# Performance work log

Measured on AMD Instinct MI355X. Metric: run time of the kernel, lower is better.

The kernel has to match this reference:

```python
import jax, jax.numpy as jnp
import numpy as np


def setup_inputs() -> dict:
    key = jax.random.key(0)
    k1, k2 = jax.random.split(key)
    B, D, H, W = 16, 256, 32, 32
    K = 2048
    z = jax.random.normal(k1, (B, D, H, W), dtype=jnp.float32)
    # EmbeddingEMA init: uniform(-1/K, 1/K); plain randn scaled works as a stand-in param
    codebook = jax.random.uniform(k2, (K, D), dtype=jnp.float32,
                                  minval=-1.0 / K, maxval=1.0 / K)
    return {"z": z, "codebook": codebook}


def reference(z, codebook):
    # z: (B, D, H, W) -> (B, H, W, D) -> (n, D)   [normalize == 'none' path]
    B, D, H, W = z.shape
    z_flat = jnp.transpose(z, (0, 2, 3, 1)).reshape(-1, D)          # (n, D)
    z_norm = z_flat
    codebook_norm = codebook                                         # (K, D)

    # squared L2 distance: ||z||^2 + ||c||^2 - 2 z c^T   -> (n, K)
    distance = (jnp.sum(z_norm * z_norm, axis=1, keepdims=True)
                + jnp.sum(codebook_norm * codebook_norm, axis=1)
                - 2.0 * jnp.matmul(z_norm, codebook_norm.T))

    vq_indices = jnp.argmin(distance, axis=1)                        # (n,)
    z_q = codebook_norm[vq_indices]                                  # gather (n, D)

    # straight-through estimator (standard VQ forward output)
    z_q_st = z_norm + jax.lax.stop_gradient(z_q - z_norm)
    out = z_q_st.reshape(B, H, W, D).transpose(0, 3, 1, 2)           # (B, D, H, W)
    return out
```

## Files before the change

### kernel.cpp

```cpp
#include <hip/hip_runtime.h>
#include <stdint.h>


#define D_    256
#define K_    2048
#define HW_   1024
#define MT    64
#define NT    256
#define KT    16
#define SPLIT 4
#define KS    (K_ / SPLIT)
#define CST   256
#define BUFSZ (KT * CST)
#define NPH   ((KS / NT) * KT)
#define NPIX  16384

__device__ __forceinline__ void gload16(const float* g, float* l) {
    auto* gp = reinterpret_cast<const __attribute__((address_space(1))) uint32_t*>(
        reinterpret_cast<uintptr_t>(g));
    auto* lp = reinterpret_cast<__attribute__((address_space(3))) uint32_t*>(
        reinterpret_cast<uintptr_t>(l));
    __builtin_amdgcn_global_load_lds(gp, lp, 16, 0, 0);
}

__device__ __forceinline__ float pw8(const float r[8]) {
    float t01 = __fadd_rn(r[0], r[1]);
    float t23 = __fadd_rn(r[2], r[3]);
    float L   = __fadd_rn(t01, t23);
    float t45 = __fadd_rn(r[4], r[5]);
    float t67 = __fadd_rn(r[6], r[7]);
    float R   = __fadd_rn(t45, t67);
    return __fadd_rn(L, R);
}

__global__ __launch_bounds__(256) void prep_k(const float* __restrict__ z,
                                              const float* __restrict__ cb,
                                              float* __restrict__ ct,
                                              float* __restrict__ An,
                                              float* __restrict__ Bn) {
    __shared__ float t[64][65];
    int tid = threadIdx.x;
    int bx  = blockIdx.x;
    if (bx < 128) {
        int k0 = (bx & 31) << 6;
        int d0 = (bx >> 5) << 6;
        #pragma unroll
        for (int it = 0; it < 4; ++it) {
            int u  = (it << 8) + tid;
            int kk = u >> 4;
            int dd = (u & 15) << 2;
            float4 v = *reinterpret_cast<const float4*>(
                cb + (size_t)(k0 + kk) * D_ + d0 + dd);
            t[kk][dd + 0] = v.x; t[kk][dd + 1] = v.y;
            t[kk][dd + 2] = v.z; t[kk][dd + 3] = v.w;
        }
        __syncthreads();
        #pragma unroll
        for (int it = 0; it < 4; ++it) {
            int u  = (it << 8) + tid;
            int dd = u >> 4;
            int kk = (u & 15) << 2;
            float4 o;
            o.x = t[kk + 0][dd]; o.y = t[kk + 1][dd];
            o.z = t[kk + 2][dd]; o.w = t[kk + 3][dd];
            *reinterpret_cast<float4*>(ct + (size_t)(d0 + dd) * K_ + k0 + kk) = o;
        }
    } else if (bx < 136) {
        int row = (bx - 128) * 256 + tid;
        const float4* p = reinterpret_cast<const float4*>(cb + (size_t)row * D_);
        float rA[8], rB[8];
        #pragma unroll
        for (int j = 0; j < 8; ++j) { rA[j] = 0.f; rB[j] = 0.f; }
        #pragma unroll
        for (int q = 0; q < 64; ++q) {
            float4 v = p[q];
            float pv[4] = {__fmul_rn(v.x, v.x), __fmul_rn(v.y, v.y),
                           __fmul_rn(v.z, v.z), __fmul_rn(v.w, v.w)};
            if (q < 32) {
                #pragma unroll
                for (int l = 0; l < 4; ++l)
                    rA[(4 * q + l) & 7] = __fadd_rn(rA[(4 * q + l) & 7], pv[l]);
            } else {
                #pragma unroll
                for (int l = 0; l < 4; ++l)
                    rB[(4 * q + l) & 7] = __fadd_rn(rB[(4 * q + l) & 7], pv[l]);
            }
        }
        Bn[row] = __fadd_rn(pw8(rA), pw8(rB));
    } else {
        int blk = bx - 136;
        int b   = blk >> 2;
        int hw0 = (blk & 3) << 8;
        const float* zb = z + (size_t)b * (D_ * HW_) + hw0 + tid;
        float rA[8], rB[8];
        #pragma unroll
        for (int j = 0; j < 8; ++j) { rA[j] = 0.f; rB[j] = 0.f; }
        #pragma unroll 8
        for (int d = 0; d < 128; ++d) {
            float v = zb[(size_t)d * HW_];
            rA[d & 7] = __fadd_rn(rA[d & 7], __fmul_rn(v, v));
        }
        #pragma unroll 8
        for (int d = 128; d < 256; ++d) {
            float v = zb[(size_t)d * HW_];
            rB[d & 7] = __fadd_rn(rB[d & 7], __fmul_rn(v, v));
        }
        An[(size_t)b * HW_ + hw0 + tid] = __fadd_rn(pw8(rA), pw8(rB));
    }
}

__global__ __launch_bounds__(256, 2) void vq_k(const float* __restrict__ z,
                                               const float* __restrict__ ct,
                                               const float* __restrict__ An,
                                               const float* __restrict__ Bn,
                                               float* __restrict__ pscore,
                                               int* __restrict__ pidx) {
    __shared__ float smem[2 * BUFSZ];
    float* rs = smem;
    int*   ri = (int*)(smem + MT * 33);

    const int tid  = threadIdx.x;
    const int lane = tid & 63;
    const int w    = tid >> 6;
    const int tn   = (tid & 7) | (w << 3);
    const int tm   = (tid >> 3) & 7;
    const int blk  = blockIdx.x;
    const int p    = blk / SPLIT;
    const int s    = blk % SPLIT;
    const int b      = p >> 4;
    const int hwbase = (p & 15) << 6;
    const float* zbase = z + (size_t)b * (D_ * HW_) + hwbase;
    const float* ctS   = ct + s * KS;

    const float* zgp = zbase + (tm << 3);

    float bs[8]; int bi[8];
    #pragma unroll
    for (int i = 0; i < 8; ++i) { bs[i] = 1e30f; bi[i] = 0; }
    float acc[8][8];
    #pragma unroll
    for (int i = 0; i < 8; ++i)
        #pragma unroll
        for (int j = 0; j < 8; ++j) acc[i][j] = 0.f;

    #define STAGE(ph)                                                         \
        do {                                                                  \
            int buf_ = (ph) & 1, kc_ = (ph) & 15, nc_ = (ph) >> 4;            \
            float* cb_ = smem + buf_ * BUFSZ;                                 \
            _Pragma("unroll")                                                 \
            for (int r = 0; r < 4; ++r) {                                     \
                int row = (w << 2) + r;                                       \
                gload16(ctS + (size_t)((kc_ << 4) + row) * K_ + nc_ * NT      \
                            + (lane << 2),                                    \
                        cb_ + row * CST);                                     \
            }                                                                 \
        } while (0)

    STAGE(0);

    for (int ph = 0; ph < NPH; ++ph) {
        __syncthreads();
        if (ph < NPH - 1) STAGE(ph + 1);
        const float* cb_ = smem + (ph & 1) * BUFSZ;
        const int kc = ph & 15;
        const float* zph = zgp + (size_t)(kc << 4) * HW_;
        #pragma unroll
        for (int d = 0; d < KT; ++d) {
            const float* zr = zph + (size_t)d * HW_;
            float4 a0 = *reinterpret_cast<const float4*>(zr);
            float4 a1 = *reinterpret_cast<const float4*>(zr + 4);
            const float* cr = cb_ + d * CST + (tn << 3);
            float4 b0 = *reinterpret_cast<const float4*>(cr);
            float4 b1 = *reinterpret_cast<const float4*>(cr + 4);
            float av[8] = {a0.x, a0.y, a0.z, a0.w, a1.x, a1.y, a1.z, a1.w};
            float bv[8] = {b0.x, b0.y, b0.z, b0.w, b1.x, b1.y, b1.z, b1.w};
            #pragma unroll
            for (int i = 0; i < 8; ++i)
                #pragma unroll
                for (int j = 0; j < 8; ++j)
                    acc[i][j] = fmaf(av[i], bv[j], acc[i][j]);
        }
        if ((ph & 15) == 15) {
            int nc = ph >> 4;
            #pragma unroll
            for (int j = 0; j < 8; ++j) {
                int ng = s * KS + nc * NT + (tn << 3) + j;
                float bn = Bn[ng];
                #pragma unroll
                for (int i = 0; i < 8; ++i) {
                    float an = An[(size_t)b * HW_ + hwbase + (tm << 3) + i];
                    float sc = __fsub_rn(__fadd_rn(an, bn),
                                         __fmul_rn(2.0f, acc[i][j]));
                    if (sc < bs[i]) { bs[i] = sc; bi[i] = ng; }
                }
            }
            #pragma unroll
            for (int i = 0; i < 8; ++i)
                #pragma unroll
                for (int j = 0; j < 8; ++j) acc[i][j] = 0.f;
        }
    }
    #undef STAGE

    __syncthreads();
    #pragma unroll
    for (int i = 0; i < 8; ++i) {
        int m = (tm << 3) + i;
        rs[m * 33 + tn] = bs[i];
        ri[m * 33 + tn] = bi[i];
    }
    __syncthreads();
    if (tid < MT) {
        int   m    = tid;
        float best = rs[m * 33];
        int   bidx = ri[m * 33];
        for (int t = 1; t < 32; ++t) {
            float sv = rs[m * 33 + t];
            int   ix = ri[m * 33 + t];
            if (sv < best || (sv == best && ix < bidx)) { best = sv; bidx = ix; }
        }
        int g = b * HW_ + hwbase + m;
        pscore[s * NPIX + g] = best;
        pidx[s * NPIX + g]   = bidx;
    }
}

__global__ __launch_bounds__(256) void fin_k(const float* __restrict__ cb,
                                             const float* __restrict__ pscore,
                                             const int* __restrict__ pidx,
                                             float* __restrict__ out) {
    __shared__ int idxs[MT];
    int tid = threadIdx.x;
    int p   = blockIdx.x;
    int b      = p >> 4;
    int hwbase = (p & 15) << 6;
    if (tid < MT) {
        int g = b * HW_ + hwbase + tid;
        float best = pscore[g];
        int   bidx = pidx[g];
        #pragma unroll
        for (int s = 1; s < SPLIT; ++s) {
            float sv = pscore[s * NPIX + g];
            int   ix = pidx[s * NPIX + g];
            if (sv < best || (sv == best && ix < bidx)) { best = sv; bidx = ix; }
        }
        idxs[tid] = bidx;
    }
    __syncthreads();
    float* obase = out + (size_t)b * (D_ * HW_) + hwbase;
    #pragma unroll
    for (int it = 0; it < 16; ++it) {
        int u  = (it << 8) + tid;
        int dd = u >> 4;
        int m4 = u & 15;
        int i0 = idxs[(m4 << 2) + 0];
        int i1 = idxs[(m4 << 2) + 1];
        int i2 = idxs[(m4 << 2) + 2];
        int i3 = idxs[(m4 << 2) + 3];
        float4 o;
        o.x = cb[(size_t)i0 * D_ + dd];
        o.y = cb[(size_t)i1 * D_ + dd];
        o.z = cb[(size_t)i2 * D_ + dd];
        o.w = cb[(size_t)i3 * D_ + dd];
        *reinterpret_cast<float4*>(obase + (size_t)dd * HW_ + (m4 << 2)) = o;
    }
}

extern "C" void kernel_launch(void* const* d_in, const int* in_sizes, int n_in,
                              void* d_out, int out_size, void* d_ws, size_t ws_size,
                              hipStream_t stream) {
    const float* z  = (const float*)d_in[0];
    const float* cb = (const float*)d_in[1];
    float* pscore = (float*)d_ws;
    int*   pidx   = (int*)(pscore + SPLIT * NPIX);
    float* An     = (float*)(pidx + SPLIT * NPIX);
    float* Bn     = An + NPIX;
    float* ct     = Bn + K_;
    float* out    = (float*)d_out;

    prep_k<<<dim3(200), dim3(256), 0, stream>>>(z, cb, ct, An, Bn);
    vq_k<<<dim3(256 * SPLIT), dim3(256), 0, stream>>>(z, ct, An, Bn, pscore, pidx);
    fin_k<<<dim3(256), dim3(256), 0, stream>>>(cb, pscore, pidx, out);
}
```

Before: 315.7 us.

## Replace LDS-staged 8x8 register tiling with per-lane 64-code accumulators reading codebook via scalar loads

Rewrites the distance kernel so each wave handles 64 pixels (one per lane) against 64 codes. Each lane holds 64 accumulators, and the codebook values are wave-uniform, so they can be read through scalar loads instead of async global-to-LDS double buffering. This removes the LDS staging, the barriers and the LDS reads in the inner loop. In exchange it raises register pressure with 512-thread blocks, and it gives up the 8x8 outer-product reuse of z loads, reducing arithmetic intensity per load.

Result: slower. 339.8 us (+7.6%).

```diff
diff --git a/kernel.cpp b/kernel.cpp
--- a/kernel.cpp
+++ b/kernel.cpp
@@ -6,22 +6,9 @@
 #define K_    2048
 #define HW_   1024
 #define MT    64
-#define NT    256
-#define KT    16
 #define SPLIT 4
 #define KS    (K_ / SPLIT)
-#define CST   256
-#define BUFSZ (KT * CST)
-#define NPH   ((KS / NT) * KT)
 #define NPIX  16384
-
-__device__ __forceinline__ void gload16(const float* g, float* l) {
-    auto* gp = reinterpret_cast<const __attribute__((address_space(1))) uint32_t*>(
-        reinterpret_cast<uintptr_t>(g));
-    auto* lp = reinterpret_cast<__attribute__((address_space(3))) uint32_t*>(
-        reinterpret_cast<uintptr_t>(l));
-    __builtin_amdgcn_global_load_lds(gp, lp, 16, 0, 0);
-}
 
 __device__ __forceinline__ float pw8(const float r[8]) {
     float t01 = __fadd_rn(r[0], r[1]);
@@ -109,119 +96,64 @@
     }
 }
 
-__global__ __launch_bounds__(256, 2) void vq_k(const float* __restrict__ z,
+__global__ __launch_bounds__(512, 2) void vq_k(const float* __restrict__ z,
                                                const float* __restrict__ ct,
                                                const float* __restrict__ An,
                                                const float* __restrict__ Bn,
                                                float* __restrict__ pscore,
                                                int* __restrict__ pidx) {
-    __shared__ float smem[2 * BUFSZ];
-    float* rs = smem;
-    int*   ri = (int*)(smem + MT * 33);
+    __shared__ float rs[512];
+    __shared__ int   ri[512];
 
     const int tid  = threadIdx.x;
     const int lane = tid & 63;
-    const int w    = tid >> 6;
-    const int tn   = (tid & 7) | (w << 3);
-    const int tm   = (tid >> 3) & 7;
+    const int wu   = __builtin_amdgcn_readfirstlane(tid >> 6);
     const int blk  = blockIdx.x;
     const int p    = blk / SPLIT;
     const int s    = blk % SPLIT;
     const int b      = p >> 4;
     const int hwbase = (p & 15) << 6;
-    const float* zbase = z + (size_t)b * (D_ * HW_) + hwbase;
-    const float* ctS   = ct + s * KS;
-
-    const float* zgp = zbase + (tm << 3);
-
-    float bs[8]; int bi[8];
+
+    const int code0 = s * KS + (wu << 6);
+    const float* zp = z + (size_t)b * (D_ * HW_) + hwbase + lane;
+    const float* cp = ct + code0;
+
+    float acc[64];
     #pragma unroll
-    for (int i = 0; i < 8; ++i) { bs[i] = 1e30f; bi[i] = 0; }
-    float acc[8][8];
+    for (int j = 0; j < 64; ++j) acc[j] = 0.f;
+
+    for (int d = 0; d < D_; ++d) {
+        float zv = zp[(size_t)d * HW_];
+        const float* cr = cp + (size_t)d * K_;
+        #pragma unroll
+        for (int j = 0; j < 64; ++j)
+            acc[j] = fmaf(zv, cr[j], acc[j]);
+    }
+
+    float an = An[(size_t)b * HW_ + hwbase + lane];
+    const float* bp = Bn + code0;
+    float best = 1e30f; int bidx = 0;
     #pragma unroll
-    for (int i = 0; i < 8; ++i)
-        #pragma unroll
-        for (int j = 0; j < 8; ++j) acc[i][j] = 0.f;
-
-    #define STAGE(ph)                                                         \
-        do {                                                                  \
-            int buf_ = (ph) & 1, kc_ = (ph) & 15, nc_ = (ph) >> 4;            \
-            float* cb_ = smem + buf_ * BUFSZ;                                 \
-            _Pragma("unroll")                                                 \
-            for (int r = 0; r < 4; ++r) {                                     \
-                int row = (w << 2) + r;                                       \
-                gload16(ctS + (size_t)((kc_ << 4) + row) * K_ + nc_ * NT      \
-                            + (lane << 2),                                    \
-                        cb_ + row * CST);                                     \
-            }                                                                 \
-        } while (0)
-
-    STAGE(0);
-
-    for (int ph = 0; ph < NPH; ++ph) {
-        __syncthreads();
-        if (ph < NPH - 1) STAGE(ph + 1);
-        const float* cb_ = smem + (ph & 1) * BUFSZ;
-        const int kc = ph & 15;
-        const float* zph = zgp + (size_t)(kc << 4) * HW_;
-        #pragma unroll
-        for (int d = 0; d < KT; ++d) {
-            const float* zr = zph + (size_t)d * HW_;
-            float4 a0 = *reinterpret_cast<const float4*>(zr);
-            float4 a1 = *reinterpret_cast<const float4*>(zr + 4);
-            const float* cr = cb_ + d * CST + (tn << 3);
-            float4 b0 = *reinterpret_cast<const float4*>(cr);
-            float4 b1 = *reinterpret_cast<const float4*>(cr + 4);
-            float av[8] = {a0.x, a0.y, a0.z, a0.w, a1.x, a1.y, a1.z, a1.w};
-            float bv[8] = {b0.x, b0.y, b0.z, b0.w, b1.x, b1.y, b1.z, b1.w};
-            #pragma unroll
-            for (int i = 0; i < 8; ++i)
-                #pragma unroll
-                for (int j = 0; j < 8; ++j)
-                    acc[i][j] = fmaf(av[i], bv[j], acc[i][j]);
-        }
-        if ((ph & 15) == 15) {
-            int nc = ph >> 4;
-            #pragma unroll
-            for (int j = 0; j < 8; ++j) {
-                int ng = s * KS + nc * NT + (tn << 3) + j;
-                float bn = Bn[ng];
-                #pragma unroll
-                for (int i = 0; i < 8; ++i) {
-                    float an = An[(size_t)b * HW_ + hwbase + (tm << 3) + i];
-                    float sc = __fsub_rn(__fadd_rn(an, bn),
-                                         __fmul_rn(2.0f, acc[i][j]));
-                    if (sc < bs[i]) { bs[i] = sc; bi[i] = ng; }
-                }
-            }
-            #pragma unroll
-            for (int i = 0; i < 8; ++i)
-                #pragma unroll
-                for (int j = 0; j < 8; ++j) acc[i][j] = 0.f;
-        }
-    }
-    #undef STAGE
-
-    __syncthreads();
-    #pragma unroll
-    for (int i = 0; i < 8; ++i) {
-        int m = (tm << 3) + i;
-        rs[m * 33 + tn] = bs[i];
-        ri[m * 33 + tn] = bi[i];
-    }
+    for (int j = 0; j < 64; ++j) {
+        float sc = __fsub_rn(__fadd_rn(an, bp[j]),
+                             __fmul_rn(2.0f, acc[j]));
+        if (sc < best) { best = sc; bidx = code0 + j; }
+    }
+
+    rs[(wu << 6) + lane] = best;
+    ri[(wu << 6) + lane] = bidx;
     __syncthreads();
     if (tid < MT) {
-        int   m    = tid;
-        float best = rs[m * 33];
-        int   bidx = ri[m * 33];
-        for (int t = 1; t < 32; ++t) {
-            float sv = rs[m * 33 + t];
-            int   ix = ri[m * 33 + t];
-            if (sv < best || (sv == best && ix < bidx)) { best = sv; bidx = ix; }
-        }
-        int g = b * HW_ + hwbase + m;
-        pscore[s * NPIX + g] = best;
-        pidx[s * NPIX + g]   = bidx;
+        float bb = rs[tid]; int bx = ri[tid];
+        #pragma unroll
+        for (int t = 1; t < 8; ++t) {
+            float sv = rs[(t << 6) + tid];
+            int   ix = ri[(t << 6) + tid];
+            if (sv < bb || (sv == bb && ix < bx)) { bb = sv; bx = ix; }
+        }
+        int g = b * HW_ + hwbase + tid;
+        pscore[s * NPIX + g] = bb;
+        pidx[s * NPIX + g]   = bx;
     }
 }
 
@@ -279,6 +211,6 @@
     float* out    = (float*)d_out;
 
     prep_k<<<dim3(200), dim3(256), 0, stream>>>(z, cb, ct, An, Bn);
-    vq_k<<<dim3(256 * SPLIT), dim3(256), 0, stream>>>(z, ct, An, Bn, pscore, pidx);
+    vq_k<<<dim3(256 * SPLIT), dim3(512), 0, stream>>>(z, ct, An, Bn, pscore, pidx);
     fin_k<<<dim3(256), dim3(256), 0, stream>>>(cb, pscore, pidx, out);
 }
```
